# Kernel optimization log

Hardware: AMD Instinct MI355X
Metric: run time of the kernel (lower is better)

The kernel has to match this reference:

```python
import jax, jax.numpy as jnp
import numpy as np

INPUT, HIDDEN, OUTPUT = 256, 512, 64
B, T = 128, 256

def gru_layer(x, W_ih, W_hh, b_ih, b_hh):
    # x: [B, T, in]; W_ih: [3H, in]; W_hh: [3H, H]; gate order r, z, n (PyTorch)
    Bv = x.shape[0]
    H = W_hh.shape[1]
    xg = jnp.einsum('bti,gi->btg', x, W_ih) + b_ih  # precompute input gates [B,T,3H]

    def step(h, xg_t):
        hg = h @ W_hh.T + b_hh
        xr, xz, xn = jnp.split(xg_t, 3, axis=-1)
        hr, hz, hn = jnp.split(hg, 3, axis=-1)
        r = jax.nn.sigmoid(xr + hr)
        z = jax.nn.sigmoid(xz + hz)
        n = jnp.tanh(xn + r * hn)
        h_new = (1.0 - z) * n + z * h
        return h_new, h_new

    h0 = jnp.zeros((Bv, H), x.dtype)
    _, ys = jax.lax.scan(step, h0, jnp.swapaxes(xg, 0, 1))  # [T,B,H]
    return jnp.swapaxes(ys, 0, 1)  # [B,T,H]

def setup_inputs() -> dict:
    key = jax.random.key(0)
    ks = jax.random.split(key, 12)
    s_in = 1.0 / np.sqrt(HIDDEN)
    inp = {
        'x': jax.random.normal(ks[0], (B, T, INPUT), dtype=jnp.float32),
        'W_ih0': jax.random.uniform(ks[1], (3 * HIDDEN, INPUT), minval=-s_in, maxval=s_in),
        'W_hh0': jax.random.uniform(ks[2], (3 * HIDDEN, HIDDEN), minval=-s_in, maxval=s_in),
        'b_ih0': jax.random.uniform(ks[3], (3 * HIDDEN,), minval=-s_in, maxval=s_in),
        'b_hh0': jax.random.uniform(ks[4], (3 * HIDDEN,), minval=-s_in, maxval=s_in),
        'W_ih1': jax.random.uniform(ks[5], (3 * HIDDEN, HIDDEN), minval=-s_in, maxval=s_in),
        'W_hh1': jax.random.uniform(ks[6], (3 * HIDDEN, HIDDEN), minval=-s_in, maxval=s_in),
        'b_ih1': jax.random.uniform(ks[7], (3 * HIDDEN,), minval=-s_in, maxval=s_in),
        'b_hh1': jax.random.uniform(ks[8], (3 * HIDDEN,), minval=-s_in, maxval=s_in),
        'W_out': jax.random.uniform(ks[9], (OUTPUT, HIDDEN), minval=-s_in, maxval=s_in),
        'b_out': jax.random.uniform(ks[10], (OUTPUT,), minval=-s_in, maxval=s_in),
    }
    return inp

def reference(x, W_ih0, W_hh0, b_ih0, b_hh0, W_ih1, W_hh1, b_ih1, b_hh1, W_out, b_out):
    h = gru_layer(x, W_ih0, W_hh0, b_ih0, b_hh0)   # layer 0
    h = gru_layer(h, W_ih1, W_hh1, b_ih1, b_hh1)   # layer 1 (dropout=0.0 -> no-op)
    last = h[:, -1, :]                              # [B, H]
    yhat = last @ W_out.T + b_out                   # [B, OUTPUT]
    return yhat
```

## Files before the change

### kernel.cpp

```cpp
#include <hip/hip_runtime.h>
#include <hip/hip_bf16.h>
#include <stdint.h>

typedef __attribute__((ext_vector_type(8))) __bf16 bf16x8;
typedef __attribute__((ext_vector_type(4))) float  floatx4;

#define T_STEPS 256
#define BATCH   128
#define HID     512

__device__ __forceinline__ float sigmoidf_(float x) { return 1.f / (1.f + __expf(-x)); }
__device__ __forceinline__ float tanhf_(float y) {
  float e = __expf(-2.f * fabsf(y));
  return copysignf((1.f - e) / (1.f + e), y);
}

template <int SLP>
__device__ __forceinline__ void pollline_(const int* base, int target) {
  while (1) {
    int v = __hip_atomic_load(base, __ATOMIC_RELAXED, __HIP_MEMORY_SCOPE_AGENT);
    if (__all(v >= target)) break;
    __builtin_amdgcn_s_sleep(SLP);
  }
  asm volatile("" ::: "memory");
}

__global__ __launch_bounds__(256) void gru_fused(
    const float* __restrict__ x,
    const float* __restrict__ Wih0, const float* __restrict__ Whh0,
    const float* __restrict__ bih0, const float* __restrict__ bhh0,
    const float* __restrict__ Wih1, const float* __restrict__ Whh1,
    const float* __restrict__ bih1, const float* __restrict__ bhh1,
    __bf16* __restrict__ h0base,
    __bf16* __restrict__ h1base,
    int* __restrict__ fl)
{
  const int tid   = threadIdx.x;
  const int layer = blockIdx.x >> 7;
  const int bg    = (blockIdx.x >> 6) & 1;
  const int g     = blockIdx.x & 63;
  const int w = tid >> 6, l = tid & 63, c = l & 15, q = l >> 4;
  const int Kin = layer ? HID : 256;
  const int KTx = Kin >> 5;
  const int KT  = KTx + 16;
  const int rowbase = bg * 64 + w * 16;
  const int jj  = g * 8 + c;

  const float* Wih = layer ? Wih1 : Wih0;
  const float* Whh = layer ? Whh1 : Whh0;
  const float* bih = layer ? bih1 : bih0;
  const float* bhh = layer ? bhh1 : bhh0;
  __bf16* hbase = layer ? h1base : h0base;

  __shared__ __bf16 ldsW[2 * 32 * 64 * 8];

  for (int cid = tid; cid < 2 * KT * 64; cid += 256) {
    int nt = cid / (KT * 64);
    int r1 = cid - nt * (KT * 64);
    int kt = r1 >> 6;
    int ll = r1 & 63;
    int cc = ll & 15, qq = ll >> 4;
    int k  = kt * 32 + qq * 8;
    int grow;
    if (nt == 0) grow = (cc < 8) ? (g * 8 + cc) : (512 + g * 8 + (cc - 8));
    else         grow = (cc < 8) ? (1024 + g * 8 + cc) : -1;
    bf16x8 v;
    if (grow >= 0) {
      const float* src = (k < Kin) ? (Wih + (size_t)grow * Kin + k)
                                   : (Whh + (size_t)grow * HID + (k - Kin));
      #pragma unroll
      for (int j = 0; j < 8; ++j) v[j] = (__bf16)src[j];
    } else {
      #pragma unroll
      for (int j = 0; j < 8; ++j) v[j] = (__bf16)0.f;
    }
    *(bf16x8*)&ldsW[((size_t)(nt * KT + kt) * 64 + ll) * 8] = v;
  }
  __syncthreads();

  bf16x8 WH[16][2];
  #pragma unroll
  for (int kt = 0; kt < 16; ++kt) {
    WH[kt][0] = *(const bf16x8*)&ldsW[((size_t)(0 * KT + KTx + kt) * 64 + l) * 8];
    WH[kt][1] = *(const bf16x8*)&ldsW[((size_t)(1 * KT + KTx + kt) * 64 + l) * 8];
  }

  float bias0, bias_nx, bias_nh;
  if (c < 8) {
    bias0   = bih[jj] + bhh[jj];
    bias_nx = bih[1024 + jj];
    bias_nh = bhh[1024 + jj];
  } else {
    int j2 = g * 8 + (c - 8);
    bias0   = bih[512 + j2] + bhh[512 + j2];
    bias_nx = 0.f; bias_nh = 0.f;
  }

  floatx4 accA[2], accB[2];
  const floatx4 zero4 = {0.f, 0.f, 0.f, 0.f};
  float hprev[4] = {0.f, 0.f, 0.f, 0.f};

  int* fpost      = fl + ((size_t)((layer * 2 + bg) * 64 + g)) * 32;
  const int* fown = fl + ((size_t)((layer * 2 + bg) * 64 + l)) * 32;
  const int* fx   = fl + ((size_t)(bg * 64 + l)) * 32;

  auto hslab = [&](int t) -> __bf16* {
    return hbase + (size_t)t * (BATCH * HID);
  };

  auto phaseX = [&](int t) {
    accA[0] = zero4; accA[1] = zero4;
    if (layer == 0) {
      const float* xp = x + ((size_t)(rowbase + c) * T_STEPS + t) * 256 + q * 8;
      for (int kt = 0; kt < 8; ++kt) {
        bf16x8 b0 = *(const bf16x8*)&ldsW[((size_t)(0 * KT + kt) * 64 + l) * 8];
        bf16x8 b1 = *(const bf16x8*)&ldsW[((size_t)(1 * KT + kt) * 64 + l) * 8];
        floatx4 u = *(const floatx4*)(xp + kt * 32);
        floatx4 v = *(const floatx4*)(xp + kt * 32 + 4);
        bf16x8 a;
        a[0] = (__bf16)u[0]; a[1] = (__bf16)u[1]; a[2] = (__bf16)u[2]; a[3] = (__bf16)u[3];
        a[4] = (__bf16)v[0]; a[5] = (__bf16)v[1]; a[6] = (__bf16)v[2]; a[7] = (__bf16)v[3];
        accA[0] = __builtin_amdgcn_mfma_f32_16x16x32_bf16(a, b0, accA[0], 0, 0, 0);
        accA[1] = __builtin_amdgcn_mfma_f32_16x16x32_bf16(a, b1, accA[1], 0, 0, 0);
      }
    } else {
      const __bf16* xp = h0base + (size_t)t * (BATCH * HID)
                       + (size_t)(rowbase + c) * HID + q * 8;
      for (int kt = 0; kt < 16; ++kt) {
        bf16x8 b0 = *(const bf16x8*)&ldsW[((size_t)(0 * KT + kt) * 64 + l) * 8];
        bf16x8 b1 = *(const bf16x8*)&ldsW[((size_t)(1 * KT + kt) * 64 + l) * 8];
        bf16x8 a = *(const bf16x8*)(xp + kt * 32);
        accA[0] = __builtin_amdgcn_mfma_f32_16x16x32_bf16(a, b0, accA[0], 0, 0, 0);
        accA[1] = __builtin_amdgcn_mfma_f32_16x16x32_bf16(a, b1, accA[1], 0, 0, 0);
      }
    }
  };

  if (layer == 1) pollline_<2>(fx, 1);
  phaseX(0);

  for (int t = 0; t < T_STEPS; ++t) {
    accB[0] = zero4; accB[1] = zero4;
    if (t > 0) {
      const __bf16* hA = hslab(t - 1) + (size_t)(rowbase + c) * HID + q * 8;
      bf16x8 hfrag[16];
      #pragma unroll
      for (int kt = 0; kt < 16; ++kt)
        hfrag[kt] = *(const bf16x8*)(hA + kt * 32);
      #pragma unroll
      for (int kt = 0; kt < 16; ++kt) {
        accB[0] = __builtin_amdgcn_mfma_f32_16x16x32_bf16(hfrag[kt], WH[kt][0], accB[0], 0, 0, 0);
        accB[1] = __builtin_amdgcn_mfma_f32_16x16x32_bf16(hfrag[kt], WH[kt][1], accB[1], 0, 0, 0);
      }
    }

    __bf16* hs = hslab(t);
    #pragma unroll
    for (int rg = 0; rg < 4; ++rg) {
      float pre0 = accA[0][rg] + accB[0][rg] + bias0;
      float zs = __shfl(pre0, (l & 48) | ((c + 8) & 15), 64);
      float r  = sigmoidf_(pre0);
      float z  = sigmoidf_(zs);
      float nn = tanhf_(accA[1][rg] + bias_nx + r * (accB[1][rg] + bias_nh));
      float hnew = (1.f - z) * nn + z * hprev[rg];
      hprev[rg] = hnew;
      unsigned short us = __builtin_bit_cast(unsigned short, (__bf16)hnew);
      int po = __shfl_xor((int)us, 1, 64);
      if (c < 8 && (c & 1) == 0) {
        uint32_t v = (uint32_t)us | ((uint32_t)po << 16);
        int row = rowbase + q * 4 + rg;
        __hip_atomic_store((uint32_t*)(hs + (size_t)row * HID + jj), v,
                           __ATOMIC_RELAXED, __HIP_MEMORY_SCOPE_AGENT);
      }
    }

    asm volatile("s_waitcnt vmcnt(0)" ::: "memory");
    __syncthreads();
    if (tid == 0)
      __hip_atomic_store(fpost, t + 1, __ATOMIC_RELAXED, __HIP_MEMORY_SCOPE_AGENT);

    if (t + 1 < T_STEPS) {
      if (layer == 1) pollline_<2>(fx, t + 2);
      phaseX(t + 1);
      pollline_<1>(fown, t + 1);
    }
  }
}

__global__ __launch_bounds__(64) void outproj(const __bf16* __restrict__ h1,
                                              const float* __restrict__ Wout,
                                              const float* __restrict__ bout,
                                              float* __restrict__ out) {
  int b = blockIdx.x, o = threadIdx.x;
  const __bf16* hr = h1 + (size_t)b * HID;
  const float*  wr = Wout + (size_t)o * HID;
  float acc = bout[o];
  for (int k = 0; k < HID; k += 8) {
    bf16x8 h8 = *(const bf16x8*)(hr + k);
    #pragma unroll
    for (int j = 0; j < 8; ++j) acc += (float)h8[j] * wr[k + j];
  }
  out[b * 64 + o] = acc;
}

extern "C" void kernel_launch(void* const* d_in, const int* in_sizes, int n_in,
                              void* d_out, int out_size, void* d_ws, size_t ws_size,
                              hipStream_t stream) {
  const float* x    = (const float*)d_in[0];
  const float* Wih0 = (const float*)d_in[1];
  const float* Whh0 = (const float*)d_in[2];
  const float* bih0 = (const float*)d_in[3];
  const float* bhh0 = (const float*)d_in[4];
  const float* Wih1 = (const float*)d_in[5];
  const float* Whh1 = (const float*)d_in[6];
  const float* bih1 = (const float*)d_in[7];
  const float* bhh1 = (const float*)d_in[8];
  const float* Wout = (const float*)d_in[9];
  const float* bout = (const float*)d_in[10];

  char* ws = (char*)d_ws;
  __bf16* h0 = (__bf16*)(ws);
  __bf16* h1 = (__bf16*)(ws + (32u << 20));
  int*    fl = (int*)(ws + (64u << 20));

  (void)hipMemsetAsync(fl, 0, 2 * 2 * 64 * 32 * 4, stream);

  gru_fused<<<256, 256, 0, stream>>>(x,
                                     Wih0, Whh0, bih0, bhh0,
                                     Wih1, Whh1, bih1, bhh1,
                                     h0, h1, fl);

  outproj<<<128, 64, 0, stream>>>(h1 + (size_t)255 * BATCH * HID,
                                  Wout, bout, (float*)d_out);
}
```

Baseline: 1.733 ms.

## Partition GRU recurrence per XCD with register-resident weights and XCD-local flags

Blocks read their hardware XCC id and claim a slot, so each XCD runs one independent ring: one layer for one quarter of the batch. The recurrent handoff then goes through an XCD-local 8-deep ring buffer whose flags are polled with L2-local sc0 loads plus buffer_inv, instead of agent-scope flags spread across all dies. Weights for the r/z/n gates are held in registers per wave, and a dedicated wave computes the gate nonlinearities from LDS-shared preactivations. A fourth wave streams layer-0 outputs to global memory for layer 1 with a lagged flag. The design relies on the hardware placing exactly 32 blocks per XCD, which is not guaranteed. Bounded polling that silently gives up hides deadlocks, and the lagged cross-layer flag risks correctness.

```diff
diff --git a/kernel.cpp b/kernel.cpp
--- a/kernel.cpp
+++ b/kernel.cpp
@@ -8,6 +8,7 @@
 #define T_STEPS 256
 #define BATCH   128
 #define HID     512
+#define POLL_CAP 2000000
 
 __device__ __forceinline__ float sigmoidf_(float x) { return 1.f / (1.f + __expf(-x)); }
 __device__ __forceinline__ float tanhf_(float y) {
@@ -15,185 +16,263 @@
   return copysignf((1.f - e) / (1.f + e), y);
 }
 
-template <int SLP>
-__device__ __forceinline__ void pollline_(const int* base, int target) {
-  while (1) {
-    int v = __hip_atomic_load(base, __ATOMIC_RELAXED, __HIP_MEMORY_SCOPE_AGENT);
-    if (__all(v >= target)) break;
-    __builtin_amdgcn_s_sleep(SLP);
-  }
-  asm volatile("" ::: "memory");
-}
-
-__global__ __launch_bounds__(256) void gru_fused(
+__device__ __forceinline__ int load_sc0(const int* p) {
+  int v;
+  asm volatile("global_load_dword %0, %1, off sc0\n\t"
+               "s_waitcnt vmcnt(0)"
+               : "=v"(v) : "v"(p) : "memory");
+  return v;
+}
+
+__global__ __launch_bounds__(256, 1) void gru_xcd(
     const float* __restrict__ x,
     const float* __restrict__ Wih0, const float* __restrict__ Whh0,
     const float* __restrict__ bih0, const float* __restrict__ bhh0,
     const float* __restrict__ Wih1, const float* __restrict__ Whh1,
     const float* __restrict__ bih1, const float* __restrict__ bhh1,
-    __bf16* __restrict__ h0base,
-    __bf16* __restrict__ h1base,
-    int* __restrict__ fl)
+    __bf16* __restrict__ h0g,
+    __bf16* __restrict__ larena,
+    int* __restrict__ claim,
+    int* __restrict__ iflags,
+    int* __restrict__ cflags)
 {
-  const int tid   = threadIdx.x;
-  const int layer = blockIdx.x >> 7;
-  const int bg    = (blockIdx.x >> 6) & 1;
-  const int g     = blockIdx.x & 63;
-  const int w = tid >> 6, l = tid & 63, c = l & 15, q = l >> 4;
-  const int Kin = layer ? HID : 256;
-  const int KTx = Kin >> 5;
-  const int KT  = KTx + 16;
-  const int rowbase = bg * 64 + w * 16;
-  const int jj  = g * 8 + c;
+  __shared__ int s_ring, s_slot;
+  __shared__ float LZ[2][16][16], LNA[2][16][16], LNB[2][16][16];
+  __shared__ uint32_t LH[2][256];
+
+  const int tid = threadIdx.x;
+  if (tid == 0) {
+    int xcc;
+    asm volatile("s_getreg_b32 %0, hwreg(HW_REG_XCC_ID)" : "=s"(xcc));
+    xcc &= 7;
+    s_ring = xcc;
+    s_slot = atomicAdd(&claim[xcc], 1);
+  }
+  __syncthreads();
+  const int  ring  = s_ring;
+  const bool valid = (s_slot < 32);
+  const int  slot  = s_slot & 31;
+  const int  layer = ring >> 2;
+  const int  bq    = ring & 3;
+  const int  w = tid >> 6, l = tid & 63, c = l & 15, q = l >> 4;
+  const int  jj0 = slot * 16;
+  const int  Kin = layer ? HID : 256;
+  const int  KTx = Kin >> 5;
 
   const float* Wih = layer ? Wih1 : Wih0;
   const float* Whh = layer ? Whh1 : Whh0;
   const float* bih = layer ? bih1 : bih0;
   const float* bhh = layer ? bhh1 : bhh0;
-  __bf16* hbase = layer ? h1base : h0base;
-
-  __shared__ __bf16 ldsW[2 * 32 * 64 * 8];
-
-  for (int cid = tid; cid < 2 * KT * 64; cid += 256) {
-    int nt = cid / (KT * 64);
-    int r1 = cid - nt * (KT * 64);
-    int kt = r1 >> 6;
-    int ll = r1 & 63;
-    int cc = ll & 15, qq = ll >> 4;
-    int k  = kt * 32 + qq * 8;
-    int grow;
-    if (nt == 0) grow = (cc < 8) ? (g * 8 + cc) : (512 + g * 8 + (cc - 8));
-    else         grow = (cc < 8) ? (1024 + g * 8 + cc) : -1;
-    bf16x8 v;
-    if (grow >= 0) {
-      const float* src = (k < Kin) ? (Wih + (size_t)grow * Kin + k)
-                                   : (Whh + (size_t)grow * HID + (k - Kin));
-      #pragma unroll
-      for (int j = 0; j < 8; ++j) v[j] = (__bf16)src[j];
+
+  __bf16* lbase = larena + (size_t)ring * 8 * 32 * HID;
+  int* ifl = iflags + ring * 32 * 32;
+  int* cfl = cflags + bq * 32 * 32;
+
+  bf16x8 Wreg[32];
+  if (w < 3) {
+    const int grow = w * HID + jj0 + c;
+    const float* wih_r = Wih + (size_t)grow * Kin;
+    const float* whh_r = Whh + (size_t)grow * HID;
+    #pragma unroll
+    for (int kt = 0; kt < 16; ++kt) {
+      const float* s = whh_r + kt * 32 + q * 8;
+      bf16x8 v;
+      #pragma unroll
+      for (int j = 0; j < 8; ++j) v[j] = (__bf16)s[j];
+      Wreg[kt] = v;
+    }
+    #pragma unroll
+    for (int kt = 0; kt < 16; ++kt) {
+      if (kt < KTx) {
+        const float* s = wih_r + kt * 32 + q * 8;
+        bf16x8 v;
+        #pragma unroll
+        for (int j = 0; j < 8; ++j) v[j] = (__bf16)s[j];
+        Wreg[16 + kt] = v;
+      }
+    }
+  }
+
+  float b_r, b_z, b_nx, b_nh;
+  {
+    int jj = jj0 + c;
+    b_r  = bih[jj] + bhh[jj];
+    b_z  = bih[HID + jj] + bhh[HID + jj];
+    b_nx = bih[2 * HID + jj];
+    b_nh = bhh[2 * HID + jj];
+  }
+
+  floatx4 accA[2], accB[2];
+  const floatx4 z4 = {0.f, 0.f, 0.f, 0.f};
+  float hprev[2][4] = {{0.f,0.f,0.f,0.f},{0.f,0.f,0.f,0.f}};
+  bool alive = valid;
+
+  auto phaseX = [&](int t) {
+    accA[0] = z4; accA[1] = z4;
+    if (layer == 0) {
+      #pragma unroll
+      for (int mt = 0; mt < 2; ++mt) {
+        int row = bq * 32 + mt * 16 + c;
+        const float* xp = x + ((size_t)row * T_STEPS + t) * 256 + q * 8;
+        #pragma unroll
+        for (int kt = 0; kt < 8; ++kt) {
+          floatx4 u = *(const floatx4*)(xp + kt * 32);
+          floatx4 v = *(const floatx4*)(xp + kt * 32 + 4);
+          bf16x8 a;
+          a[0]=(__bf16)u[0]; a[1]=(__bf16)u[1]; a[2]=(__bf16)u[2]; a[3]=(__bf16)u[3];
+          a[4]=(__bf16)v[0]; a[5]=(__bf16)v[1]; a[6]=(__bf16)v[2]; a[7]=(__bf16)v[3];
+          accA[mt] = __builtin_amdgcn_mfma_f32_16x16x32_bf16(a, Wreg[16 + kt], accA[mt], 0, 0, 0);
+        }
+      }
     } else {
       #pragma unroll
-      for (int j = 0; j < 8; ++j) v[j] = (__bf16)0.f;
-    }
-    *(bf16x8*)&ldsW[((size_t)(nt * KT + kt) * 64 + ll) * 8] = v;
-  }
-  __syncthreads();
-
-  bf16x8 WH[16][2];
-  #pragma unroll
-  for (int kt = 0; kt < 16; ++kt) {
-    WH[kt][0] = *(const bf16x8*)&ldsW[((size_t)(0 * KT + KTx + kt) * 64 + l) * 8];
-    WH[kt][1] = *(const bf16x8*)&ldsW[((size_t)(1 * KT + KTx + kt) * 64 + l) * 8];
-  }
-
-  float bias0, bias_nx, bias_nh;
-  if (c < 8) {
-    bias0   = bih[jj] + bhh[jj];
-    bias_nx = bih[1024 + jj];
-    bias_nh = bhh[1024 + jj];
-  } else {
-    int j2 = g * 8 + (c - 8);
-    bias0   = bih[512 + j2] + bhh[512 + j2];
-    bias_nx = 0.f; bias_nh = 0.f;
-  }
-
-  floatx4 accA[2], accB[2];
-  const floatx4 zero4 = {0.f, 0.f, 0.f, 0.f};
-  float hprev[4] = {0.f, 0.f, 0.f, 0.f};
-
-  int* fpost      = fl + ((size_t)((layer * 2 + bg) * 64 + g)) * 32;
-  const int* fown = fl + ((size_t)((layer * 2 + bg) * 64 + l)) * 32;
-  const int* fx   = fl + ((size_t)(bg * 64 + l)) * 32;
-
-  auto hslab = [&](int t) -> __bf16* {
-    return hbase + (size_t)t * (BATCH * HID);
+      for (int mt = 0; mt < 2; ++mt) {
+        int row = bq * 32 + mt * 16 + c;
+        const __bf16* xp = h0g + ((size_t)t * BATCH + row) * HID + q * 8;
+        #pragma unroll
+        for (int kt = 0; kt < 16; ++kt) {
+          bf16x8 a = *(const bf16x8*)(xp + kt * 32);
+          accA[mt] = __builtin_amdgcn_mfma_f32_16x16x32_bf16(a, Wreg[16 + kt], accA[mt], 0, 0, 0);
+        }
+      }
+    }
   };
 
-  auto phaseX = [&](int t) {
-    accA[0] = zero4; accA[1] = zero4;
-    if (layer == 0) {
-      const float* xp = x + ((size_t)(rowbase + c) * T_STEPS + t) * 256 + q * 8;
-      for (int kt = 0; kt < 8; ++kt) {
-        bf16x8 b0 = *(const bf16x8*)&ldsW[((size_t)(0 * KT + kt) * 64 + l) * 8];
-        bf16x8 b1 = *(const bf16x8*)&ldsW[((size_t)(1 * KT + kt) * 64 + l) * 8];
-        floatx4 u = *(const floatx4*)(xp + kt * 32);
-        floatx4 v = *(const floatx4*)(xp + kt * 32 + 4);
-        bf16x8 a;
-        a[0] = (__bf16)u[0]; a[1] = (__bf16)u[1]; a[2] = (__bf16)u[2]; a[3] = (__bf16)u[3];
-        a[4] = (__bf16)v[0]; a[5] = (__bf16)v[1]; a[6] = (__bf16)v[2]; a[7] = (__bf16)v[3];
-        accA[0] = __builtin_amdgcn_mfma_f32_16x16x32_bf16(a, b0, accA[0], 0, 0, 0);
-        accA[1] = __builtin_amdgcn_mfma_f32_16x16x32_bf16(a, b1, accA[1], 0, 0, 0);
-      }
-    } else {
-      const __bf16* xp = h0base + (size_t)t * (BATCH * HID)
-                       + (size_t)(rowbase + c) * HID + q * 8;
+  auto phaseH = [&](int tprev) {
+    accB[0] = z4; accB[1] = z4;
+    const __bf16* hb = lbase + (size_t)(tprev & 7) * 32 * HID;
+    #pragma unroll
+    for (int mt = 0; mt < 2; ++mt) {
+      const __bf16* hp = hb + (size_t)(mt * 16 + c) * HID + q * 8;
+      #pragma unroll
       for (int kt = 0; kt < 16; ++kt) {
-        bf16x8 b0 = *(const bf16x8*)&ldsW[((size_t)(0 * KT + kt) * 64 + l) * 8];
-        bf16x8 b1 = *(const bf16x8*)&ldsW[((size_t)(1 * KT + kt) * 64 + l) * 8];
-        bf16x8 a = *(const bf16x8*)(xp + kt * 32);
-        accA[0] = __builtin_amdgcn_mfma_f32_16x16x32_bf16(a, b0, accA[0], 0, 0, 0);
-        accA[1] = __builtin_amdgcn_mfma_f32_16x16x32_bf16(a, b1, accA[1], 0, 0, 0);
+        bf16x8 a = *(const bf16x8*)(hp + kt * 32);
+        accB[mt] = __builtin_amdgcn_mfma_f32_16x16x32_bf16(a, Wreg[kt], accB[mt], 0, 0, 0);
       }
     }
   };
 
-  if (layer == 1) pollline_<2>(fx, 1);
-  phaseX(0);
+  auto polli = [&](int target) {
+    if (!alive) return;
+    const int* p = ifl + (l & 31) * 32;
+    int it = 0;
+    while (1) {
+      int v = load_sc0(p);
+      if (__all(v >= target)) break;
+      if (++it > POLL_CAP) { alive = false; break; }
+      __builtin_amdgcn_s_sleep(1);
+    }
+  };
+  auto pollc = [&](int target) {
+    if (!alive) return;
+    const int* p = cfl + (l & 31) * 32;
+    int it = 0;
+    while (1) {
+      int v = __hip_atomic_load(p, __ATOMIC_RELAXED, __HIP_MEMORY_SCOPE_AGENT);
+      if (__all(v >= target)) break;
+      if (++it > POLL_CAP) { alive = false; break; }
+      __builtin_amdgcn_s_sleep(1);
+    }
+  };
+
+  if (w < 3) {
+    if (layer == 1) pollc(1);
+    phaseX(0);
+  }
 
   for (int t = 0; t < T_STEPS; ++t) {
-    accB[0] = zero4; accB[1] = zero4;
-    if (t > 0) {
-      const __bf16* hA = hslab(t - 1) + (size_t)(rowbase + c) * HID + q * 8;
-      bf16x8 hfrag[16];
-      #pragma unroll
-      for (int kt = 0; kt < 16; ++kt)
-        hfrag[kt] = *(const bf16x8*)(hA + kt * 32);
-      #pragma unroll
-      for (int kt = 0; kt < 16; ++kt) {
-        accB[0] = __builtin_amdgcn_mfma_f32_16x16x32_bf16(hfrag[kt], WH[kt][0], accB[0], 0, 0, 0);
-        accB[1] = __builtin_amdgcn_mfma_f32_16x16x32_bf16(hfrag[kt], WH[kt][1], accB[1], 0, 0, 0);
-      }
-    }
-
-    __bf16* hs = hslab(t);
-    #pragma unroll
-    for (int rg = 0; rg < 4; ++rg) {
-      float pre0 = accA[0][rg] + accB[0][rg] + bias0;
-      float zs = __shfl(pre0, (l & 48) | ((c + 8) & 15), 64);
-      float r  = sigmoidf_(pre0);
-      float z  = sigmoidf_(zs);
-      float nn = tanhf_(accA[1][rg] + bias_nx + r * (accB[1][rg] + bias_nh));
-      float hnew = (1.f - z) * nn + z * hprev[rg];
-      hprev[rg] = hnew;
-      unsigned short us = __builtin_bit_cast(unsigned short, (__bf16)hnew);
-      int po = __shfl_xor((int)us, 1, 64);
-      if (c < 8 && (c & 1) == 0) {
-        uint32_t v = (uint32_t)us | ((uint32_t)po << 16);
-        int row = rowbase + q * 4 + rg;
-        __hip_atomic_store((uint32_t*)(hs + (size_t)row * HID + jj), v,
+    if (w < 3) {
+      if (t > 0) {
+        polli(t);
+        asm volatile("buffer_inv" ::: "memory");
+        phaseH(t - 1);
+      } else {
+        accB[0] = z4; accB[1] = z4;
+      }
+      if (w == 1) {
+        #pragma unroll
+        for (int mt = 0; mt < 2; ++mt)
+          #pragma unroll
+          for (int rg = 0; rg < 4; ++rg)
+            LZ[mt][q * 4 + rg][c] = accA[mt][rg] + accB[mt][rg];
+      } else if (w == 2) {
+        #pragma unroll
+        for (int mt = 0; mt < 2; ++mt)
+          #pragma unroll
+          for (int rg = 0; rg < 4; ++rg) {
+            LNA[mt][q * 4 + rg][c] = accA[mt][rg];
+            LNB[mt][q * 4 + rg][c] = accB[mt][rg];
+          }
+      }
+    }
+    __syncthreads();
+
+    if (w == 0) {
+      __bf16* hs = lbase + (size_t)(t & 7) * 32 * HID;
+      #pragma unroll
+      for (int mt = 0; mt < 2; ++mt) {
+        #pragma unroll
+        for (int rg = 0; rg < 4; ++rg) {
+          int row = q * 4 + rg;
+          float r  = sigmoidf_(accA[mt][rg] + accB[mt][rg] + b_r);
+          float zv = sigmoidf_(LZ[mt][row][c] + b_z);
+          float nn = tanhf_(LNA[mt][row][c] + b_nx + r * (LNB[mt][row][c] + b_nh));
+          float h  = (1.f - zv) * nn + zv * hprev[mt][rg];
+          hprev[mt][rg] = h;
+          unsigned short us = __builtin_bit_cast(unsigned short, (__bf16)h);
+          int po = __shfl_xor((int)us, 1, 64);
+          if ((c & 1) == 0) {
+            uint32_t pv = (uint32_t)us | ((uint32_t)po << 16);
+            int lr = mt * 16 + row;
+            *(uint32_t*)(hs + (size_t)lr * HID + jj0 + c) = pv;
+            LH[t & 1][((mt * 4 + q) * 4 + rg) * 8 + (c >> 1)] = pv;
+          }
+        }
+      }
+      asm volatile("s_waitcnt vmcnt(0)" ::: "memory");
+      *(volatile int*)(ifl + slot * 32) = t + 1;
+    }
+    __syncthreads();
+
+    if (w == 3 && layer == 0 && valid) {
+      uint32_t d[4];
+      #pragma unroll
+      for (int i = 0; i < 4; ++i) d[i] = LH[t & 1][l * 4 + i];
+      #pragma unroll
+      for (int i = 0; i < 4; ++i) {
+        int di = l * 4 + i;
+        int mt = di >> 7, qq = (di >> 5) & 3, rg = (di >> 3) & 3, cp = di & 7;
+        int gr = bq * 32 + mt * 16 + qq * 4 + rg;
+        uint32_t* gp = (uint32_t*)(h0g + ((size_t)t * BATCH + gr) * HID + jj0 + cp * 2);
+        __hip_atomic_store(gp, d[i], __ATOMIC_RELAXED, __HIP_MEMORY_SCOPE_AGENT);
+      }
+      if (t < T_STEPS - 1) {
+        asm volatile("s_waitcnt vmcnt(9)" ::: "memory");
+        if (t >= 1)
+          __hip_atomic_store(cfl + slot * 32, t - 1,
+                             __ATOMIC_RELAXED, __HIP_MEMORY_SCOPE_AGENT);
+      } else {
+        asm volatile("s_waitcnt vmcnt(0)" ::: "memory");
+        __hip_atomic_store(cfl + slot * 32, T_STEPS,
                            __ATOMIC_RELAXED, __HIP_MEMORY_SCOPE_AGENT);
       }
     }
 
-    asm volatile("s_waitcnt vmcnt(0)" ::: "memory");
-    __syncthreads();
-    if (tid == 0)
-      __hip_atomic_store(fpost, t + 1, __ATOMIC_RELAXED, __HIP_MEMORY_SCOPE_AGENT);
-
-    if (t + 1 < T_STEPS) {
-      if (layer == 1) pollline_<2>(fx, t + 2);
+    if (w < 3 && t + 1 < T_STEPS) {
+      if (layer == 1) pollc(t + 2);
       phaseX(t + 1);
-      pollline_<1>(fown, t + 1);
-    }
-  }
-}
-
-__global__ __launch_bounds__(64) void outproj(const __bf16* __restrict__ h1,
+    }
+  }
+}
+
+__global__ __launch_bounds__(64) void outproj(const __bf16* __restrict__ larena,
                                               const float* __restrict__ Wout,
                                               const float* __restrict__ bout,
                                               float* __restrict__ out) {
   int b = blockIdx.x, o = threadIdx.x;
-  const __bf16* hr = h1 + (size_t)b * HID;
-  const float*  wr = Wout + (size_t)o * HID;
+  int ring = 4 + (b >> 5);
+  const __bf16* hr = larena + ((size_t)ring * 8 + 7) * 32 * HID + (size_t)(b & 31) * HID;
+  const float* wr = Wout + (size_t)o * HID;
   float acc = bout[o];
   for (int k = 0; k < HID; k += 8) {
     bf16x8 h8 = *(const bf16x8*)(hr + k);
@@ -219,17 +298,18 @@
   const float* bout = (const float*)d_in[10];
 
   char* ws = (char*)d_ws;
-  __bf16* h0 = (__bf16*)(ws);
-  __bf16* h1 = (__bf16*)(ws + (32u << 20));
-  int*    fl = (int*)(ws + (64u << 20));
-
-  (void)hipMemsetAsync(fl, 0, 2 * 2 * 64 * 32 * 4, stream);
-
-  gru_fused<<<256, 256, 0, stream>>>(x,
-                                     Wih0, Whh0, bih0, bhh0,
-                                     Wih1, Whh1, bih1, bhh1,
-                                     h0, h1, fl);
-
-  outproj<<<128, 64, 0, stream>>>(h1 + (size_t)255 * BATCH * HID,
-                                  Wout, bout, (float*)d_out);
-}
+  __bf16* h0g = (__bf16*)ws;
+  __bf16* lar = (__bf16*)(ws + 33554432);
+  int* claim  = (int*)(ws + 35651584);
+  int* ifl    = (int*)(ws + 35651584 + 1024);
+  int* cfl    = (int*)(ws + 35651584 + 1024 + 32768);
+
+  (void)hipMemsetAsync(ws + 35651584, 0, 65536, stream);
+
+  gru_xcd<<<256, 256, 0, stream>>>(x,
+                                   Wih0, Whh0, bih0, bhh0,
+                                   Wih1, Whh1, bih1, bhh1,
+                                   h0g, lar, claim, ifl, cfl);
+
+  outproj<<<128, 64, 0, stream>>>(lar, Wout, bout, (float*)d_out);
+}
```

Result: slower. 3.310 ms (+91.0%).
